# Kernel tuning notes

Measured on AMD Instinct MI355X. Metric: run time of the kernel, lower is better.

The kernel has to match this reference:

```python
import jax, jax.numpy as jnp
import numpy as np

B, S, DIN, D = 16, 1024, 64, 64

def setup_inputs() -> dict:
    key = jax.random.key(0)
    kx, kq, kk, kv, kaK, kaV = jax.random.split(key, 6)
    w_scale = 1.0 / np.sqrt(DIN)
    x = jax.random.normal(kx, (B, S, DIN), dtype=jnp.float32)
    Wq = jax.random.normal(kq, (DIN, D), dtype=jnp.float32) * w_scale
    Wk = jax.random.normal(kk, (DIN, D), dtype=jnp.float32) * w_scale
    Wv = jax.random.normal(kv, (DIN, D), dtype=jnp.float32) * w_scale
    # relative-position bias tables alpha_K/alpha_V: [S, S, D]
    alpha_K = jax.random.normal(kaK, (S, S, D), dtype=jnp.float32) * 0.02
    alpha_V = jax.random.normal(kaV, (S, S, D), dtype=jnp.float32) * 0.02
    return {"x": x, "Wq": Wq, "Wk": Wk, "Wv": Wv,
            "alpha_K": alpha_K, "alpha_V": alpha_V}

def reference(x, Wq, Wk, Wv, alpha_K, alpha_V):
    # Relation-aware self-attention (Shaw et al. style), vectorized form of
    # the original per-query loop:
    #   score[b,i,j] = q[b,i] . (k[b,j] + alpha_K[i,j]) / sqrt(D)
    #   z[b,i]       = sum_j softmax_j(score)[b,i,j] * (v[b,j] + alpha_V[i,j])
    d = Wq.shape[1]
    inv_sqrt_d = 1.0 / np.sqrt(d)
    q = jnp.einsum('bsf,fd->bsd', x, Wq)
    k = jnp.einsum('bsf,fd->bsd', x, Wk)
    v = jnp.einsum('bsf,fd->bsd', x, Wv)
    scores = (jnp.einsum('bid,bjd->bij', q, k)
              + jnp.einsum('bid,ijd->bij', q, alpha_K)) * inv_sqrt_d
    attn = jax.nn.softmax(scores, axis=-1)  # [B, S, S]
    z = (jnp.einsum('bij,bjd->bid', attn, v)
         + jnp.einsum('bij,ijd->bid', attn, alpha_V))
    return z, attn
```

## Files before the change

kernel.cpp:

```cpp
#include <hip/hip_runtime.h>
#include <hip/hip_fp16.h>
#include <hip/hip_bf16.h>


typedef unsigned short u16;
typedef __attribute__((ext_vector_type(8))) short bhalf8;
typedef __attribute__((ext_vector_type(4))) float fx4;

__device__ __forceinline__ short b16(float f) {
  __hip_bfloat16 h = __float2bfloat16(f);
  return *reinterpret_cast<short*>(&h);
}

__device__ __forceinline__ bhalf8 pack8(float4 a, float4 b) {
  bhalf8 r;
  r[0] = b16(a.x); r[1] = b16(a.y); r[2] = b16(a.z); r[3] = b16(a.w);
  r[4] = b16(b.x); r[5] = b16(b.y); r[6] = b16(b.z); r[7] = b16(b.w);
  return r;
}

__global__ __launch_bounds__(256) void k_proj(
    const float* __restrict__ x, const float* __restrict__ Wq,
    const float* __restrict__ Wk, const float* __restrict__ Wv,
    u16* __restrict__ qbf, u16* __restrict__ kbf, float* __restrict__ vf)
{
  __shared__ float wl[3 * 4096];
  const int t = threadIdx.x;
  for (int c = t; c < 4096; c += 256) {
    wl[c] = Wq[c]; wl[4096 + c] = Wk[c]; wl[8192 + c] = Wv[c];
  }
  __syncthreads();
  const int row = blockIdx.x * 64 + (t >> 2);
  const int dbase = (t & 3) * 16;
  float xr[64];
  const float4* xp = (const float4*)(x + (size_t)row * 64);
#pragma unroll
  for (int c = 0; c < 16; ++c) {
    float4 v = xp[c];
    xr[4*c] = v.x; xr[4*c+1] = v.y; xr[4*c+2] = v.z; xr[4*c+3] = v.w;
  }
  float aq[16], ak[16], av[16];
#pragma unroll
  for (int m = 0; m < 16; ++m) { aq[m] = 0.f; ak[m] = 0.f; av[m] = 0.f; }
#pragma unroll
  for (int f = 0; f < 64; ++f) {
    const float xv = xr[f];
    const float* wq = wl + f * 64 + dbase;
#pragma unroll
    for (int m = 0; m < 16; ++m) {
      aq[m] = fmaf(xv, wq[m], aq[m]);
      ak[m] = fmaf(xv, wq[4096 + m], ak[m]);
      av[m] = fmaf(xv, wq[8192 + m], av[m]);
    }
  }
  union { u16 u[16]; uint4 q[2]; } pq, pk;
#pragma unroll
  for (int m = 0; m < 16; ++m) { pq.u[m] = (u16)b16(aq[m]); pk.u[m] = (u16)b16(ak[m]); }
  const size_t o = (size_t)row * 64 + dbase;
  *(uint4*)(qbf + o) = pq.q[0]; *(uint4*)(qbf + o + 8) = pq.q[1];
  *(uint4*)(kbf + o) = pk.q[0]; *(uint4*)(kbf + o + 8) = pk.q[1];
  float4* vo = (float4*)(vf + o);
  vo[0] = make_float4(av[0], av[1], av[2], av[3]);
  vo[1] = make_float4(av[4], av[5], av[6], av[7]);
  vo[2] = make_float4(av[8], av[9], av[10], av[11]);
  vo[3] = make_float4(av[12], av[13], av[14], av[15]);
}

__global__ __launch_bounds__(256) void k_qk(
    const u16* __restrict__ qbf, const u16* __restrict__ kbf, __half* __restrict__ qkw)
{
  const int t = threadIdx.x, l = t & 63, w = t >> 6;
  const int b = blockIdx.x & 15, it = blockIdx.x >> 4;
  const int lr = l & 15, lg = l >> 4;
  const int i0 = it * 64 + w * 16;
  const u16* qp = qbf + (size_t)(b * 1024 + i0 + lr) * 64 + lg * 8;
  bhalf8 a0 = *(const bhalf8*)(qp);
  bhalf8 a1 = *(const bhalf8*)(qp + 32);
  for (int jt = 0; jt < 64; ++jt) {
    const int j0 = jt * 16;
    const u16* kp = kbf + (size_t)(b * 1024 + j0 + lr) * 64 + lg * 8;
    bhalf8 b0 = *(const bhalf8*)(kp);
    bhalf8 b1 = *(const bhalf8*)(kp + 32);
    fx4 acc = {0.f, 0.f, 0.f, 0.f};
    acc = __builtin_amdgcn_mfma_f32_16x16x32_bf16(a0, b0, acc, 0, 0, 0);
    acc = __builtin_amdgcn_mfma_f32_16x16x32_bf16(a1, b1, acc, 0, 0, 0);
#pragma unroll
    for (int r = 0; r < 4; ++r) {
      const int i = i0 + lg * 4 + r;
      qkw[((size_t)i * 16 + b) * 1024 + j0 + lr] = __float2half(acc[r]);
    }
  }
}

#define SLD2 516
#define PADJ 40
__global__ __launch_bounds__(256, 4) void k_core(
    const float* __restrict__ aK, const float* __restrict__ aV,
    const u16* __restrict__ qbf, const __half* __restrict__ qkw,
    float* __restrict__ attn_out, float* __restrict__ za)
{
  __shared__ __align__(16) float sl[16 * SLD2];
  __shared__ __align__(16) u16 vt[64 * PADJ];
  __shared__ float stats[64];
  const int i = blockIdx.x;
  const int t = threadIdx.x, l = t & 63, w = t >> 6;
  const int lr = l & 15, lg = l >> 4;

  const u16* qp = qbf + (size_t)(lr * 1024 + i) * 64 + lg * 8;
  bhalf8 a0 = *(const bhalf8*)(qp);
  bhalf8 a1 = *(const bhalf8*)(qp + 32);

  fx4 zacc = {0.f, 0.f, 0.f, 0.f};

  for (int h = 0; h < 2; ++h) {
    for (int tt = 0; tt < 8; ++tt) {
      const int j0 = (w + tt * 4) * 16;
      const float* ap = aK + ((size_t)i * 1024 + h * 512 + j0 + lr) * 64 + lg * 8;
      float4 c0 = *(const float4*)(ap);
      float4 c1 = *(const float4*)(ap + 4);
      float4 c2 = *(const float4*)(ap + 32);
      float4 c3 = *(const float4*)(ap + 36);
      fx4 acc = {0.f, 0.f, 0.f, 0.f};
      acc = __builtin_amdgcn_mfma_f32_16x16x32_bf16(a0, pack8(c0, c1), acc, 0, 0, 0);
      acc = __builtin_amdgcn_mfma_f32_16x16x32_bf16(a1, pack8(c2, c3), acc, 0, 0, 0);
#pragma unroll
      for (int r = 0; r < 4; ++r)
        sl[(lg * 4 + r) * SLD2 + j0 + lr] = acc[r];
    }
    __syncthreads();

    if (h == 0) {
#pragma unroll
      for (int rr = 0; rr < 4; ++rr) {
        const int row = w * 4 + rr;
        float* rp = sl + row * SLD2;
        uint4 qv = *(const uint4*)(qkw + ((size_t)i * 16 + row) * 1024 + l * 8);
        const __half2* hh = (const __half2*)&qv;
        float2 f0 = __half22float2(hh[0]);
        float2 f1 = __half22float2(hh[1]);
        float2 f2 = __half22float2(hh[2]);
        float2 f3 = __half22float2(hh[3]);
        float4 x0 = *(const float4*)(rp + l * 8);
        float4 x1 = *(const float4*)(rp + l * 8 + 4);
        float v8[8] = {x0.x + f0.x, x0.y + f0.y, x0.z + f1.x, x0.w + f1.y,
                       x1.x + f2.x, x1.y + f2.y, x1.z + f3.x, x1.w + f3.y};
        float mx = -3.0e30f;
#pragma unroll
        for (int c = 0; c < 8; ++c) mx = fmaxf(mx, v8[c]);
#pragma unroll
        for (int off = 32; off; off >>= 1) mx = fmaxf(mx, __shfl_xor(mx, off));
        float e8[8]; float sum = 0.f;
#pragma unroll
        for (int c = 0; c < 8; ++c) { e8[c] = __expf((v8[c] - mx) * 0.125f); sum += e8[c]; }
        float* ao = attn_out + ((size_t)row * 1024 + i) * 1024;
        *(float4*)(ao + l * 8)     = make_float4(e8[0], e8[1], e8[2], e8[3]);
        *(float4*)(ao + l * 8 + 4) = make_float4(e8[4], e8[5], e8[6], e8[7]);
        bhalf8 eb;
#pragma unroll
        for (int c = 0; c < 8; ++c) eb[c] = b16(e8[c]);
        *(bhalf8*)((u16*)rp + l * 8) = eb;
#pragma unroll
        for (int off = 32; off; off >>= 1) sum += __shfl_xor(sum, off);
        if (l == 0) { stats[row] = mx; stats[16 + row] = sum; }
      }
    } else {
#pragma unroll
      for (int rr = 0; rr < 4; ++rr) {
        const int row = w * 4 + rr;
        float* rp = sl + row * SLD2;
        uint4 qv = *(const uint4*)(qkw + ((size_t)i * 16 + row) * 1024 + 512 + l * 8);
        const __half2* hh = (const __half2*)&qv;
        float2 f0 = __half22float2(hh[0]);
        float2 f1 = __half22float2(hh[1]);
        float2 f2 = __half22float2(hh[2]);
        float2 f3 = __half22float2(hh[3]);
        float4 x0 = *(const float4*)(rp + l * 8);
        float4 x1 = *(const float4*)(rp + l * 8 + 4);
        float v8[8] = {x0.x + f0.x, x0.y + f0.y, x0.z + f1.x, x0.w + f1.y,
                       x1.x + f2.x, x1.y + f2.y, x1.z + f3.x, x1.w + f3.y};
        float mx = -3.0e30f;
#pragma unroll
        for (int c = 0; c < 8; ++c) mx = fmaxf(mx, v8[c]);
#pragma unroll
        for (int off = 32; off; off >>= 1) mx = fmaxf(mx, __shfl_xor(mx, off));
        const float m1 = stats[row];
        const float m  = fmaxf(m1, mx);
        const float corr = __expf((m1 - m) * 0.125f);
        float e8[8]; float sum = 0.f;
#pragma unroll
        for (int c = 0; c < 8; ++c) { e8[c] = __expf((v8[c] - m) * 0.125f); sum += e8[c]; }
        bhalf8 eb;
#pragma unroll
        for (int c = 0; c < 8; ++c) eb[c] = b16(e8[c]);
        *(bhalf8*)((u16*)rp + l * 8) = eb;
#pragma unroll
        for (int off = 32; off; off >>= 1) sum += __shfl_xor(sum, off);
        const float inv = 1.0f / (stats[16 + row] * corr + sum);
        float* ao = attn_out + ((size_t)row * 1024 + i) * 1024 + 512;
        *(float4*)(ao + l * 8)     = make_float4(e8[0]*inv, e8[1]*inv, e8[2]*inv, e8[3]*inv);
        *(float4*)(ao + l * 8 + 4) = make_float4(e8[4]*inv, e8[5]*inv, e8[6]*inv, e8[7]*inv);
        if (l == 0) { stats[32 + row] = corr; stats[48 + row] = inv; }
      }
    }
    __syncthreads();

    if (h == 1) {
#pragma unroll
      for (int r = 0; r < 4; ++r) zacc[r] *= stats[32 + lg * 4 + r];
    }
    const int jj = l >> 2;
    const int cc = (l & 3) * 4;
    const float* avbase = aV + ((size_t)i * 1024 + h * 512) * 64 + w * 16 + cc;
    float4 pa = *(const float4*)(avbase + (size_t)jj * 64);
    float4 pb = *(const float4*)(avbase + (size_t)(jj + 16) * 64);
    for (int it = 0; it < 16; ++it) {
      float4 ca = pa, cb = pb;
      if (it < 15) {
        const float* nb = avbase + (size_t)((it + 1) * 32) * 64;
        pa = *(const float4*)(nb + (size_t)jj * 64);
        pb = *(const float4*)(nb + (size_t)(jj + 16) * 64);
      }
      u16* v0 = vt + (size_t)(w * 16 + cc) * PADJ + jj;
      v0[0 * PADJ]      = (u16)b16(ca.x);
      v0[1 * PADJ]      = (u16)b16(ca.y);
      v0[2 * PADJ]      = (u16)b16(ca.z);
      v0[3 * PADJ]      = (u16)b16(ca.w);
      v0[0 * PADJ + 16] = (u16)b16(cb.x);
      v0[1 * PADJ + 16] = (u16)b16(cb.y);
      v0[2 * PADJ + 16] = (u16)b16(cb.z);
      v0[3 * PADJ + 16] = (u16)b16(cb.w);
      bhalf8 ea = *(const bhalf8*)((const u16*)(sl + (size_t)lr * SLD2) + it * 32 + lg * 8);
      bhalf8 bv = *(const bhalf8*)(vt + (size_t)(w * 16 + lr) * PADJ + lg * 8);
      zacc = __builtin_amdgcn_mfma_f32_16x16x32_bf16(ea, bv, zacc, 0, 0, 0);
    }
    __syncthreads();
  }

#pragma unroll
  for (int r = 0; r < 4; ++r) {
    const int b = lg * 4 + r;
    za[((size_t)i * 16 + b) * 64 + w * 16 + lr] = zacc[r] * stats[48 + b];
  }

#pragma unroll
  for (int rr = 0; rr < 4; ++rr) {
    const int row = w * 4 + rr;
    const float f = stats[32 + row] * stats[48 + row];
    float* ao = attn_out + ((size_t)row * 1024 + i) * 1024;
    float4 u0 = *(const float4*)(ao + l * 8);
    float4 u1 = *(const float4*)(ao + l * 8 + 4);
    *(float4*)(ao + l * 8)     = make_float4(u0.x*f, u0.y*f, u0.z*f, u0.w*f);
    *(float4*)(ao + l * 8 + 4) = make_float4(u1.x*f, u1.y*f, u1.z*f, u1.w*f);
  }
}

__global__ __launch_bounds__(256) void k_zv(
    const float* __restrict__ attn, const float* __restrict__ vf,
    const float* __restrict__ za, float* __restrict__ zout)
{
  __shared__ __align__(16) u16 vt[64 * 40];
  const int t = threadIdx.x, l = t & 63, w = t >> 6;
  const int b = blockIdx.x & 15, it = blockIdx.x >> 4;
  const int lr = l & 15, lg = l >> 4;
  const int iw = it * 64 + w * 16;
  fx4 acc[4];
#pragma unroll
  for (int n = 0; n < 4; ++n) acc[n] = (fx4){0.f, 0.f, 0.f, 0.f};
  const int jl = t >> 3;
  const int c0 = (t & 7) * 8;
  for (int ks = 0; ks < 32; ++ks) {
    const int j0 = ks * 32;
    const float* vp = vf + (size_t)(b * 1024 + j0 + jl) * 64 + c0;
    float4 v0 = *(const float4*)(vp);
    float4 v1 = *(const float4*)(vp + 4);
    __syncthreads();
    vt[(c0 + 0) * 40 + jl] = (u16)b16(v0.x);
    vt[(c0 + 1) * 40 + jl] = (u16)b16(v0.y);
    vt[(c0 + 2) * 40 + jl] = (u16)b16(v0.z);
    vt[(c0 + 3) * 40 + jl] = (u16)b16(v0.w);
    vt[(c0 + 4) * 40 + jl] = (u16)b16(v1.x);
    vt[(c0 + 5) * 40 + jl] = (u16)b16(v1.y);
    vt[(c0 + 6) * 40 + jl] = (u16)b16(v1.z);
    vt[(c0 + 7) * 40 + jl] = (u16)b16(v1.w);
    __syncthreads();
    const float* apr = attn + (size_t)(b * 1024 + iw + lr) * 1024 + j0 + lg * 8;
    float4 t0 = *(const float4*)(apr);
    float4 t1 = *(const float4*)(apr + 4);
    bhalf8 af = pack8(t0, t1);
#pragma unroll
    for (int n = 0; n < 4; ++n) {
      bhalf8 bf = *(const bhalf8*)(vt + (n * 16 + lr) * 40 + lg * 8);
      acc[n] = __builtin_amdgcn_mfma_f32_16x16x32_bf16(af, bf, acc[n], 0, 0, 0);
    }
  }
#pragma unroll
  for (int n = 0; n < 4; ++n) {
#pragma unroll
    for (int r = 0; r < 4; ++r) {
      const int i = iw + lg * 4 + r;
      const int dd = n * 16 + lr;
      zout[((size_t)b * 1024 + i) * 64 + dd] = acc[n][r] + za[((size_t)i * 16 + b) * 64 + dd];
    }
  }
}

extern "C" void kernel_launch(void* const* d_in, const int* in_sizes, int n_in,
                              void* d_out, int out_size, void* d_ws, size_t ws_size,
                              hipStream_t stream)
{
  const float* x  = (const float*)d_in[0];
  const float* Wq = (const float*)d_in[1];
  const float* Wk = (const float*)d_in[2];
  const float* Wv = (const float*)d_in[3];
  const float* aK = (const float*)d_in[4];
  const float* aV = (const float*)d_in[5];
  float* zout = (float*)d_out;
  float* attn_out = zout + (size_t)16 * 1024 * 64;

  char* ws = (char*)d_ws;
  u16*    qbf = (u16*)(ws);
  u16*    kbf = (u16*)(ws + (size_t)2  * 1024 * 1024);
  float*  vf  = (float*)(ws + (size_t)4  * 1024 * 1024);
  float*  za  = (float*)(ws + (size_t)8  * 1024 * 1024);
  __half* qkw = (__half*)(ws + (size_t)12 * 1024 * 1024);

  hipLaunchKernelGGL(k_proj, dim3(256),  dim3(256), 0, stream, x, Wq, Wk, Wv, qbf, kbf, vf);
  hipLaunchKernelGGL(k_qk,   dim3(256),  dim3(256), 0, stream, qbf, kbf, qkw);
  hipLaunchKernelGGL(k_core, dim3(1024), dim3(256), 0, stream, aK, aV, qbf, qkw, attn_out, za);
  hipLaunchKernelGGL(k_zv,   dim3(256),  dim3(256), 0, stream, attn_out, vf, za, zout);
}
```

Baseline: 226.0 us.

## Software-pipeline global loads across kernels and drop attn rescale re-read pass

Adds explicit multi-stage register prefetching of K, alpha_K, alpha_V, V and attn tiles in k_qk, k_core and k_zv to hide global load latency. k_core keeps the first-half exponentials in bf16 registers and writes the normalized first half directly, so it no longer reads back and rescales attn_out in a second pass. k_zv is reshaped to 1024 blocks of 16 rows with one MFMA accumulator per wave, raising parallelism. In exchange, register pressure rises, and the first-half attn values are now rounded through bf16 before normalization, which costs accuracy.

```diff
diff --git a/kernel.cpp b/kernel.cpp
--- a/kernel.cpp
+++ b/kernel.cpp
@@ -10,6 +10,9 @@
 __device__ __forceinline__ short b16(float f) {
   __hip_bfloat16 h = __float2bfloat16(f);
   return *reinterpret_cast<short*>(&h);
+}
+__device__ __forceinline__ float bf2f(short s) {
+  union { unsigned u; float f; } v; v.u = ((unsigned)(u16)s) << 16; return v.f;
 }
 
 __device__ __forceinline__ bhalf8 pack8(float4 a, float4 b) {
@@ -70,25 +73,35 @@
     const u16* __restrict__ qbf, const u16* __restrict__ kbf, __half* __restrict__ qkw)
 {
   const int t = threadIdx.x, l = t & 63, w = t >> 6;
-  const int b = blockIdx.x & 15, it = blockIdx.x >> 4;
+  const int bq = blockIdx.x & 15, it = blockIdx.x >> 4;
   const int lr = l & 15, lg = l >> 4;
   const int i0 = it * 64 + w * 16;
-  const u16* qp = qbf + (size_t)(b * 1024 + i0 + lr) * 64 + lg * 8;
+  const u16* qp = qbf + (size_t)(bq * 1024 + i0 + lr) * 64 + lg * 8;
   bhalf8 a0 = *(const bhalf8*)(qp);
   bhalf8 a1 = *(const bhalf8*)(qp + 32);
-  for (int jt = 0; jt < 64; ++jt) {
-    const int j0 = jt * 16;
-    const u16* kp = kbf + (size_t)(b * 1024 + j0 + lr) * 64 + lg * 8;
-    bhalf8 b0 = *(const bhalf8*)(kp);
-    bhalf8 b1 = *(const bhalf8*)(kp + 32);
+  auto ldK = [&](int jt, bhalf8& b0, bhalf8& b1) {
+    const u16* kp = kbf + (size_t)(bq * 1024 + jt * 16 + lr) * 64 + lg * 8;
+    b0 = *(const bhalf8*)(kp);
+    b1 = *(const bhalf8*)(kp + 32);
+  };
+  auto doK = [&](int jt, bhalf8 b0, bhalf8 b1) {
     fx4 acc = {0.f, 0.f, 0.f, 0.f};
     acc = __builtin_amdgcn_mfma_f32_16x16x32_bf16(a0, b0, acc, 0, 0, 0);
     acc = __builtin_amdgcn_mfma_f32_16x16x32_bf16(a1, b1, acc, 0, 0, 0);
 #pragma unroll
     for (int r = 0; r < 4; ++r) {
       const int i = i0 + lg * 4 + r;
-      qkw[((size_t)i * 16 + b) * 1024 + j0 + lr] = __float2half(acc[r]);
-    }
+      qkw[((size_t)i * 16 + bq) * 1024 + jt * 16 + lr] = __float2half(acc[r]);
+    }
+  };
+  bhalf8 k0a, k0b, k1a, k1b, k2a, k2b, k3a, k3b;
+  ldK(0, k0a, k0b); ldK(1, k1a, k1b); ldK(2, k2a, k2b); ldK(3, k3a, k3b);
+#pragma unroll
+  for (int jt = 0; jt < 64; jt += 4) {
+    doK(jt + 0, k0a, k0b); if (jt + 4 < 64) ldK(jt + 4, k0a, k0b);
+    doK(jt + 1, k1a, k1b); if (jt + 5 < 64) ldK(jt + 5, k1a, k1b);
+    doK(jt + 2, k2a, k2b); if (jt + 6 < 64) ldK(jt + 6, k2a, k2b);
+    doK(jt + 3, k3a, k3b); if (jt + 7 < 64) ldK(jt + 7, k3a, k3b);
   }
 }
 
@@ -105,27 +118,46 @@
   const int i = blockIdx.x;
   const int t = threadIdx.x, l = t & 63, w = t >> 6;
   const int lr = l & 15, lg = l >> 4;
+  const int jj = l >> 2;
+  const int cc = (l & 3) * 4;
 
   const u16* qp = qbf + (size_t)(lr * 1024 + i) * 64 + lg * 8;
   bhalf8 a0 = *(const bhalf8*)(qp);
   bhalf8 a1 = *(const bhalf8*)(qp + 32);
 
   fx4 zacc = {0.f, 0.f, 0.f, 0.f};
-
+  bhalf8 e1b[4];
+
+#pragma unroll
   for (int h = 0; h < 2; ++h) {
-    for (int tt = 0; tt < 8; ++tt) {
+    uint4 qv[4];
+#pragma unroll
+    for (int rr = 0; rr < 4; ++rr)
+      qv[rr] = *(const uint4*)(qkw + ((size_t)i * 16 + w * 4 + rr) * 1024 + h * 512 + l * 8);
+
+    const float* base = aK + ((size_t)i * 1024 + h * 512 + lr) * 64 + lg * 8;
+    auto ldA = [&](int tt, float4* c) {
+      const float* p = base + (size_t)((w + tt * 4) * 16) * 64;
+      c[0] = *(const float4*)(p);
+      c[1] = *(const float4*)(p + 4);
+      c[2] = *(const float4*)(p + 32);
+      c[3] = *(const float4*)(p + 36);
+    };
+    auto doA = [&](int tt, const float4* c) {
+      fx4 acc = {0.f, 0.f, 0.f, 0.f};
+      acc = __builtin_amdgcn_mfma_f32_16x16x32_bf16(a0, pack8(c[0], c[1]), acc, 0, 0, 0);
+      acc = __builtin_amdgcn_mfma_f32_16x16x32_bf16(a1, pack8(c[2], c[3]), acc, 0, 0, 0);
       const int j0 = (w + tt * 4) * 16;
-      const float* ap = aK + ((size_t)i * 1024 + h * 512 + j0 + lr) * 64 + lg * 8;
-      float4 c0 = *(const float4*)(ap);
-      float4 c1 = *(const float4*)(ap + 4);
-      float4 c2 = *(const float4*)(ap + 32);
-      float4 c3 = *(const float4*)(ap + 36);
-      fx4 acc = {0.f, 0.f, 0.f, 0.f};
-      acc = __builtin_amdgcn_mfma_f32_16x16x32_bf16(a0, pack8(c0, c1), acc, 0, 0, 0);
-      acc = __builtin_amdgcn_mfma_f32_16x16x32_bf16(a1, pack8(c2, c3), acc, 0, 0, 0);
 #pragma unroll
       for (int r = 0; r < 4; ++r)
         sl[(lg * 4 + r) * SLD2 + j0 + lr] = acc[r];
+    };
+    float4 cA[4], cB[4];
+    ldA(0, cA); ldA(1, cB);
+#pragma unroll
+    for (int tt = 0; tt < 8; tt += 2) {
+      doA(tt, cA);     if (tt + 2 < 8) ldA(tt + 2, cA);
+      doA(tt + 1, cB); if (tt + 3 < 8) ldA(tt + 3, cB);
     }
     __syncthreads();
 
@@ -134,8 +166,7 @@
       for (int rr = 0; rr < 4; ++rr) {
         const int row = w * 4 + rr;
         float* rp = sl + row * SLD2;
-        uint4 qv = *(const uint4*)(qkw + ((size_t)i * 16 + row) * 1024 + l * 8);
-        const __half2* hh = (const __half2*)&qv;
+        const __half2* hh = (const __half2*)&qv[rr];
         float2 f0 = __half22float2(hh[0]);
         float2 f1 = __half22float2(hh[1]);
         float2 f2 = __half22float2(hh[2]);
@@ -152,13 +183,11 @@
         float e8[8]; float sum = 0.f;
 #pragma unroll
         for (int c = 0; c < 8; ++c) { e8[c] = __expf((v8[c] - mx) * 0.125f); sum += e8[c]; }
-        float* ao = attn_out + ((size_t)row * 1024 + i) * 1024;
-        *(float4*)(ao + l * 8)     = make_float4(e8[0], e8[1], e8[2], e8[3]);
-        *(float4*)(ao + l * 8 + 4) = make_float4(e8[4], e8[5], e8[6], e8[7]);
         bhalf8 eb;
 #pragma unroll
         for (int c = 0; c < 8; ++c) eb[c] = b16(e8[c]);
         *(bhalf8*)((u16*)rp + l * 8) = eb;
+        e1b[rr] = eb;
 #pragma unroll
         for (int off = 32; off; off >>= 1) sum += __shfl_xor(sum, off);
         if (l == 0) { stats[row] = mx; stats[16 + row] = sum; }
@@ -168,8 +197,7 @@
       for (int rr = 0; rr < 4; ++rr) {
         const int row = w * 4 + rr;
         float* rp = sl + row * SLD2;
-        uint4 qv = *(const uint4*)(qkw + ((size_t)i * 16 + row) * 1024 + 512 + l * 8);
-        const __half2* hh = (const __half2*)&qv;
+        const __half2* hh = (const __half2*)&qv[rr];
         float2 f0 = __half22float2(hh[0]);
         float2 f1 = __half22float2(hh[1]);
         float2 f2 = __half22float2(hh[2]);
@@ -196,9 +224,15 @@
 #pragma unroll
         for (int off = 32; off; off >>= 1) sum += __shfl_xor(sum, off);
         const float inv = 1.0f / (stats[16 + row] * corr + sum);
-        float* ao = attn_out + ((size_t)row * 1024 + i) * 1024 + 512;
-        *(float4*)(ao + l * 8)     = make_float4(e8[0]*inv, e8[1]*inv, e8[2]*inv, e8[3]*inv);
-        *(float4*)(ao + l * 8 + 4) = make_float4(e8[4]*inv, e8[5]*inv, e8[6]*inv, e8[7]*inv);
+        float* ao1 = attn_out + ((size_t)row * 1024 + i) * 1024 + 512;
+        *(float4*)(ao1 + l * 8)     = make_float4(e8[0]*inv, e8[1]*inv, e8[2]*inv, e8[3]*inv);
+        *(float4*)(ao1 + l * 8 + 4) = make_float4(e8[4]*inv, e8[5]*inv, e8[6]*inv, e8[7]*inv);
+        const float f = corr * inv;
+        float* ao0 = attn_out + ((size_t)row * 1024 + i) * 1024;
+        *(float4*)(ao0 + l * 8)     = make_float4(bf2f(e1b[rr][0])*f, bf2f(e1b[rr][1])*f,
+                                                  bf2f(e1b[rr][2])*f, bf2f(e1b[rr][3])*f);
+        *(float4*)(ao0 + l * 8 + 4) = make_float4(bf2f(e1b[rr][4])*f, bf2f(e1b[rr][5])*f,
+                                                  bf2f(e1b[rr][6])*f, bf2f(e1b[rr][7])*f);
         if (l == 0) { stats[32 + row] = corr; stats[48 + row] = inv; }
       }
     }
@@ -208,30 +242,36 @@
 #pragma unroll
       for (int r = 0; r < 4; ++r) zacc[r] *= stats[32 + lg * 4 + r];
     }
-    const int jj = l >> 2;
-    const int cc = (l & 3) * 4;
     const float* avbase = aV + ((size_t)i * 1024 + h * 512) * 64 + w * 16 + cc;
-    float4 pa = *(const float4*)(avbase + (size_t)jj * 64);
-    float4 pb = *(const float4*)(avbase + (size_t)(jj + 16) * 64);
-    for (int it = 0; it < 16; ++it) {
-      float4 ca = pa, cb = pb;
-      if (it < 15) {
-        const float* nb = avbase + (size_t)((it + 1) * 32) * 64;
-        pa = *(const float4*)(nb + (size_t)jj * 64);
-        pb = *(const float4*)(nb + (size_t)(jj + 16) * 64);
-      }
-      u16* v0 = vt + (size_t)(w * 16 + cc) * PADJ + jj;
-      v0[0 * PADJ]      = (u16)b16(ca.x);
-      v0[1 * PADJ]      = (u16)b16(ca.y);
-      v0[2 * PADJ]      = (u16)b16(ca.z);
-      v0[3 * PADJ]      = (u16)b16(ca.w);
-      v0[0 * PADJ + 16] = (u16)b16(cb.x);
-      v0[1 * PADJ + 16] = (u16)b16(cb.y);
-      v0[2 * PADJ + 16] = (u16)b16(cb.z);
-      v0[3 * PADJ + 16] = (u16)b16(cb.w);
-      bhalf8 ea = *(const bhalf8*)((const u16*)(sl + (size_t)lr * SLD2) + it * 32 + lg * 8);
-      bhalf8 bv = *(const bhalf8*)(vt + (size_t)(w * 16 + lr) * PADJ + lg * 8);
+    u16* vtw = vt + (size_t)(w * 16 + cc) * PADJ + jj;
+    const u16* vtr = vt + (size_t)(w * 16 + lr) * PADJ + lg * 8;
+    const u16* slr = (const u16*)(sl + (size_t)lr * SLD2);
+    auto ldC = [&](int it, float4& pa, float4& pb) {
+      const float* nb = avbase + (size_t)(it * 32) * 64;
+      pa = *(const float4*)(nb + (size_t)jj * 64);
+      pb = *(const float4*)(nb + (size_t)(jj + 16) * 64);
+    };
+    auto doC = [&](int it, float4 ca, float4 cb) {
+      vtw[0 * PADJ]      = (u16)b16(ca.x);
+      vtw[1 * PADJ]      = (u16)b16(ca.y);
+      vtw[2 * PADJ]      = (u16)b16(ca.z);
+      vtw[3 * PADJ]      = (u16)b16(ca.w);
+      vtw[0 * PADJ + 16] = (u16)b16(cb.x);
+      vtw[1 * PADJ + 16] = (u16)b16(cb.y);
+      vtw[2 * PADJ + 16] = (u16)b16(cb.z);
+      vtw[3 * PADJ + 16] = (u16)b16(cb.w);
+      bhalf8 ea = *(const bhalf8*)(slr + it * 32 + lg * 8);
+      bhalf8 bv = *(const bhalf8*)(vtr);
       zacc = __builtin_amdgcn_mfma_f32_16x16x32_bf16(ea, bv, zacc, 0, 0, 0);
+    };
+    float4 p0a, p0b, p1a, p1b, p2a, p2b, p3a, p3b;
+    ldC(0, p0a, p0b); ldC(1, p1a, p1b); ldC(2, p2a, p2b); ldC(3, p3a, p3b);
+#pragma unroll
+    for (int it = 0; it < 16; it += 4) {
+      doC(it + 0, p0a, p0b); if (it + 4 < 16) ldC(it + 4, p0a, p0b);
+      doC(it + 1, p1a, p1b); if (it + 5 < 16) ldC(it + 5, p1a, p1b);
+      doC(it + 2, p2a, p2b); if (it + 6 < 16) ldC(it + 6, p2a, p2b);
+      doC(it + 3, p3a, p3b); if (it + 7 < 16) ldC(it + 7, p3a, p3b);
     }
     __syncthreads();
   }
@@ -241,67 +281,67 @@
     const int b = lg * 4 + r;
     za[((size_t)i * 16 + b) * 64 + w * 16 + lr] = zacc[r] * stats[48 + b];
   }
-
-#pragma unroll
-  for (int rr = 0; rr < 4; ++rr) {
-    const int row = w * 4 + rr;
-    const float f = stats[32 + row] * stats[48 + row];
-    float* ao = attn_out + ((size_t)row * 1024 + i) * 1024;
-    float4 u0 = *(const float4*)(ao + l * 8);
-    float4 u1 = *(const float4*)(ao + l * 8 + 4);
-    *(float4*)(ao + l * 8)     = make_float4(u0.x*f, u0.y*f, u0.z*f, u0.w*f);
-    *(float4*)(ao + l * 8 + 4) = make_float4(u1.x*f, u1.y*f, u1.z*f, u1.w*f);
-  }
 }
 
 __global__ __launch_bounds__(256) void k_zv(
     const float* __restrict__ attn, const float* __restrict__ vf,
     const float* __restrict__ za, float* __restrict__ zout)
 {
-  __shared__ __align__(16) u16 vt[64 * 40];
+  __shared__ __align__(16) u16 vt[64 * PADJ];
   const int t = threadIdx.x, l = t & 63, w = t >> 6;
-  const int b = blockIdx.x & 15, it = blockIdx.x >> 4;
+  const int b = blockIdx.x & 15, it16 = blockIdx.x >> 4;
   const int lr = l & 15, lg = l >> 4;
-  const int iw = it * 64 + w * 16;
-  fx4 acc[4];
-#pragma unroll
-  for (int n = 0; n < 4; ++n) acc[n] = (fx4){0.f, 0.f, 0.f, 0.f};
-  const int jl = t >> 3;
-  const int c0 = (t & 7) * 8;
-  for (int ks = 0; ks < 32; ++ks) {
-    const int j0 = ks * 32;
-    const float* vp = vf + (size_t)(b * 1024 + j0 + jl) * 64 + c0;
-    float4 v0 = *(const float4*)(vp);
-    float4 v1 = *(const float4*)(vp + 4);
-    __syncthreads();
-    vt[(c0 + 0) * 40 + jl] = (u16)b16(v0.x);
-    vt[(c0 + 1) * 40 + jl] = (u16)b16(v0.y);
-    vt[(c0 + 2) * 40 + jl] = (u16)b16(v0.z);
-    vt[(c0 + 3) * 40 + jl] = (u16)b16(v0.w);
-    vt[(c0 + 4) * 40 + jl] = (u16)b16(v1.x);
-    vt[(c0 + 5) * 40 + jl] = (u16)b16(v1.y);
-    vt[(c0 + 6) * 40 + jl] = (u16)b16(v1.z);
-    vt[(c0 + 7) * 40 + jl] = (u16)b16(v1.w);
-    __syncthreads();
-    const float* apr = attn + (size_t)(b * 1024 + iw + lr) * 1024 + j0 + lg * 8;
-    float4 t0 = *(const float4*)(apr);
-    float4 t1 = *(const float4*)(apr + 4);
+  const int i0 = it16 * 16;
+  const int jj = l >> 2;
+  const int cc = (l & 3) * 4;
+  const float* vbase = vf + (size_t)b * 65536 + w * 16 + cc;
+  const float* abase = attn + ((size_t)b * 1024 + i0 + lr) * 1024 + lg * 8;
+  float zr[4];
+#pragma unroll
+  for (int r = 0; r < 4; ++r)
+    zr[r] = za[((size_t)(i0 + lg * 4 + r) * 16 + b) * 64 + w * 16 + lr];
+  fx4 acc = {0.f, 0.f, 0.f, 0.f};
+  u16* vtw = vt + (size_t)(w * 16 + cc) * PADJ + jj;
+  const u16* vtr = vt + (size_t)(w * 16 + lr) * PADJ + lg * 8;
+  auto ldV = [&](int jt, float4& pa, float4& pb) {
+    const float* nb = vbase + (size_t)(jt * 32) * 64;
+    pa = *(const float4*)(nb + (size_t)jj * 64);
+    pb = *(const float4*)(nb + (size_t)(jj + 16) * 64);
+  };
+  auto ldAt = [&](int jt, float4& t0, float4& t1) {
+    const float* p = abase + jt * 32;
+    t0 = *(const float4*)(p);
+    t1 = *(const float4*)(p + 4);
+  };
+  auto doT = [&](float4 va, float4 vb, float4 t0, float4 t1) {
+    vtw[0 * PADJ]      = (u16)b16(va.x);
+    vtw[1 * PADJ]      = (u16)b16(va.y);
+    vtw[2 * PADJ]      = (u16)b16(va.z);
+    vtw[3 * PADJ]      = (u16)b16(va.w);
+    vtw[0 * PADJ + 16] = (u16)b16(vb.x);
+    vtw[1 * PADJ + 16] = (u16)b16(vb.y);
+    vtw[2 * PADJ + 16] = (u16)b16(vb.z);
+    vtw[3 * PADJ + 16] = (u16)b16(vb.w);
     bhalf8 af = pack8(t0, t1);
-#pragma unroll
-    for (int n = 0; n < 4; ++n) {
-      bhalf8 bf = *(const bhalf8*)(vt + (n * 16 + lr) * 40 + lg * 8);
-      acc[n] = __builtin_amdgcn_mfma_f32_16x16x32_bf16(af, bf, acc[n], 0, 0, 0);
-    }
-  }
-#pragma unroll
-  for (int n = 0; n < 4; ++n) {
-#pragma unroll
-    for (int r = 0; r < 4; ++r) {
-      const int i = iw + lg * 4 + r;
-      const int dd = n * 16 + lr;
-      zout[((size_t)b * 1024 + i) * 64 + dd] = acc[n][r] + za[((size_t)i * 16 + b) * 64 + dd];
-    }
-  }
+    bhalf8 bv = *(const bhalf8*)(vtr);
+    acc = __builtin_amdgcn_mfma_f32_16x16x32_bf16(af, bv, acc, 0, 0, 0);
+  };
+  float4 v0a, v0b, v1a, v1b, v2a, v2b, v3a, v3b;
+  float4 a0_, a1_, b0_, b1_, c0_, c1_, d0_, d1_;
+  ldV(0, v0a, v0b); ldAt(0, a0_, a1_);
+  ldV(1, v1a, v1b); ldAt(1, b0_, b1_);
+  ldV(2, v2a, v2b); ldAt(2, c0_, c1_);
+  ldV(3, v3a, v3b); ldAt(3, d0_, d1_);
+#pragma unroll
+  for (int jt = 0; jt < 32; jt += 4) {
+    doT(v0a, v0b, a0_, a1_); if (jt + 4 < 32) { ldV(jt + 4, v0a, v0b); ldAt(jt + 4, a0_, a1_); }
+    doT(v1a, v1b, b0_, b1_); if (jt + 5 < 32) { ldV(jt + 5, v1a, v1b); ldAt(jt + 5, b0_, b1_); }
+    doT(v2a, v2b, c0_, c1_); if (jt + 6 < 32) { ldV(jt + 6, v2a, v2b); ldAt(jt + 6, c0_, c1_); }
+    doT(v3a, v3b, d0_, d1_); if (jt + 7 < 32) { ldV(jt + 7, v3a, v3b); ldAt(jt + 7, d0_, d1_); }
+  }
+#pragma unroll
+  for (int r = 0; r < 4; ++r)
+    zout[((size_t)b * 1024 + i0 + lg * 4 + r) * 64 + w * 16 + lr] = acc[r] + zr[r];
 }
 
 extern "C" void kernel_launch(void* const* d_in, const int* in_sizes, int n_in,
@@ -327,5 +367,5 @@
   hipLaunchKernelGGL(k_proj, dim3(256),  dim3(256), 0, stream, x, Wq, Wk, Wv, qbf, kbf, vf);
   hipLaunchKernelGGL(k_qk,   dim3(256),  dim3(256), 0, stream, qbf, kbf, qkw);
   hipLaunchKernelGGL(k_core, dim3(1024), dim3(256), 0, stream, aK, aV, qbf, qkw, attn_out, za);
-  hipLaunchKernelGGL(k_zv,   dim3(256),  dim3(256), 0, stream, attn_out, vf, za, zout);
-}
+  hipLaunchKernelGGL(k_zv,   dim3(1024), dim3(256), 0, stream, attn_out, vf, za, zout);
+}
```

Result: faster. 206.7 us (-8.5%).
